# Performance work log

Measured on AMD Instinct MI355X. Metric: run time of the kernel, lower is better.

## Reference

```python
import jax, jax.numpy as jnp
import numpy as np

N_NODES = 50000


def _gcn_norm(edge_index, num_nodes):
    # PyG GCNConv default: add self-loops, symmetric normalization D^-1/2 A D^-1/2
    row, col = edge_index[0], edge_index[1]
    loop = jnp.arange(num_nodes, dtype=edge_index.dtype)
    row = jnp.concatenate([row, loop])
    col = jnp.concatenate([col, loop])
    deg = jax.ops.segment_sum(jnp.ones_like(col, dtype=jnp.float32), col,
                              num_segments=num_nodes)
    deg_inv_sqrt = jnp.where(deg > 0, jax.lax.rsqrt(deg), 0.0)
    norm = deg_inv_sqrt[row] * deg_inv_sqrt[col]  # [E + N]
    return row, col, norm


def _gcn_conv(x, row, col, norm, W, b):
    h = x @ W                                   # [N, out]
    msg = h[row] * norm[:, None]                # gather + scale, [E+N, out]
    out = jax.ops.segment_sum(msg, col, num_segments=x.shape[0])  # scatter-add
    return out + b


def setup_inputs() -> dict:
    key = jax.random.key(0)
    k_x, k_e, k_w1, k_w2 = jax.random.split(key, 4)
    n, e, d = N_NODES, 800000, 64
    x = jax.random.normal(k_x, (n, d), dtype=jnp.float32)
    edge_index = jax.random.randint(k_e, (2, e), 0, n, dtype=jnp.int64)
    # Glorot init like PyG's Linear inside GCNConv (bias separate, zero-init here as randn-small)
    s1 = (6.0 / (d + d)) ** 0.5
    W1 = jax.random.uniform(k_w1, (d, d), jnp.float32, -s1, s1)
    W2 = jax.random.uniform(k_w2, (d, d), jnp.float32, -s1, s1)
    b1 = jnp.zeros((d,), jnp.float32)
    b2 = jnp.zeros((d,), jnp.float32)
    return {"x": x, "edge_index": edge_index, "W1": W1, "b1": b1, "W2": W2, "b2": b2}


def reference(x, edge_index, W1, b1, W2, b2):
    row, col, norm = _gcn_norm(edge_index, x.shape[0])
    h = _gcn_conv(x, row, col, norm, W1, b1)   # layer 1: in -> out
    h = _gcn_conv(h, row, col, norm, W2, b2)   # layer 2: out -> out
    return h
```

## Files before the change

### kernel.cpp

```cpp
#include <hip/hip_runtime.h>
#include <hip/hip_fp16.h>

#define DD 64
#define BSH 6
#define BNODES 64
#define NSUB 8
#define SCAP 256
#define BCAP 1536

__global__ __launch_bounds__(256) void k_zero(int4* __restrict__ p, int n4) {
    int i = blockIdx.x * 256 + threadIdx.x;
    if (i < n4) p[i] = make_int4(0, 0, 0, 0);
}

__global__ __launch_bounds__(256) void k_fill3(const int* __restrict__ rowi,
                                               const int* __restrict__ coli,
                                               int* __restrict__ cur,
                                               unsigned int* __restrict__ pk, int E) {
    int i = blockIdx.x * 256 + threadIdx.x;
    if (i < E) {
        int c = coli[i];
        int idx = (c >> BSH) * NSUB + (blockIdx.x & (NSUB - 1));
        int p = atomicAdd(&cur[idx * 16], 1);
        if (p < SCAP)
            pk[(size_t)idx * SCAP + p] =
                (unsigned int)rowi[i] | ((unsigned int)(c & (BNODES - 1)) << 16);
    }
}

__global__ __launch_bounds__(256) void k_bsort(const int* __restrict__ cur,
                                               const unsigned int* __restrict__ pk,
                                               int* __restrict__ off_s,
                                               int* __restrict__ off_e,
                                               float* __restrict__ dis,
                                               int* __restrict__ srt, int n) {
    __shared__ unsigned int stage[NSUB * SCAP];
    __shared__ int cnt[BNODES];
    __shared__ int cbase[BNODES];
    __shared__ int sb8[NSUB + 1];
    int t = threadIdx.x;
    int b = blockIdx.x;

    if (t < BNODES) cnt[t] = 0;
    if (t < NSUB) {
        int v = cur[(b * NSUB + t) * 16];
        if (v > SCAP) v = SCAP;
        int x = v;
#pragma unroll
        for (int d = 1; d < NSUB; d <<= 1) {
            int u = __shfl_up(x, d, NSUB);
            if ((t & (NSUB - 1)) >= d) x += u;
        }
        sb8[t + 1] = x;
        if (t == 0) sb8[0] = 0;
    }
    __syncthreads();
    int tot = sb8[NSUB];

#pragma unroll
    for (int s = 0; s < NSUB; ++s) {
        int c0 = sb8[s], len = sb8[s + 1] - c0;
        const unsigned int* src = pk + ((size_t)b * NSUB + s) * SCAP;
        for (int i = t; i < len; i += 256) stage[c0 + i] = src[i];
    }
    __syncthreads();

    for (int i = t; i < tot; i += 256) atomicAdd(&cnt[stage[i] >> 16], 1);
    __syncthreads();

    if (t < BNODES) {
        int v = cnt[t], x = v;
#pragma unroll
        for (int d = 1; d < 64; d <<= 1) {
            int u = __shfl_up(x, d);
            if (t >= d) x += u;
        }
        int excl = x - v;
        cbase[t] = excl;
        int c = b * BNODES + t;
        if (c < n) {
            off_s[c] = b * BCAP + excl;
            off_e[c] = b * BCAP + excl + v;
            dis[c] = rsqrtf((float)(v + 1));
        }
    }
    __syncthreads();

    int sbeg = b * BCAP;
    for (int i = t; i < tot; i += 256) {
        unsigned int k = stage[i];
        int pos = atomicAdd(&cbase[k >> 16], 1);
        srt[sbeg + pos] = (int)(k & 0xFFFFu);
    }
}

__global__ __launch_bounds__(64) void k_mm(const float* __restrict__ X,
                                           const float* __restrict__ W,
                                           const float* __restrict__ dis,
                                           __half* __restrict__ H, int n) {
    int lane  = threadIdx.x;
    int tile  = blockIdx.x >> 1;
    int jbase = (blockIdx.x & 1) * 32;
    int r     = tile * 64 + lane;
    int rc    = min(r, n - 1);

    const float4* X4 = (const float4*)X;
    float acc[32];
#pragma unroll
    for (int j = 0; j < 32; ++j) acc[j] = 0.f;

#pragma unroll 1
    for (int kc = 0; kc < 16; ++kc) {
        float4 xv = X4[(size_t)rc * 16 + kc];
        const float* W0 = W + (kc * 4) * 64 + jbase;
#pragma unroll
        for (int u = 0; u < 4; ++u) {
            float xk = (u == 0) ? xv.x : (u == 1) ? xv.y : (u == 2) ? xv.z : xv.w;
            const float* Wk = W0 + u * 64;
#pragma unroll
            for (int j = 0; j < 32; ++j)
                acc[j] = fmaf(xk, Wk[j], acc[j]);
        }
    }
    if (r < n) {
        float d = dis[r];
        __half2 hh[16];
#pragma unroll
        for (int q = 0; q < 16; ++q)
            hh[q] = __floats2half2_rn(acc[2 * q] * d, acc[2 * q + 1] * d);
        uint4* dst = (uint4*)(H + (size_t)r * DD + jbase);
        const uint4* src = (const uint4*)hh;
#pragma unroll
        for (int q = 0; q < 4; ++q) dst[q] = src[q];
    }
}

__global__ __launch_bounds__(256) void k_agg(const int* __restrict__ off_s,
                                             const int* __restrict__ off_e,
                                             const int* __restrict__ srt,
                                             const float* __restrict__ dis,
                                             const __half* __restrict__ hs,
                                             const float* __restrict__ bias,
                                             float* __restrict__ out, int n) {
    int lane = threadIdx.x & 63;
    int j    = lane & 31;
    int hsel = lane >> 5;
    int c = __builtin_amdgcn_readfirstlane(blockIdx.x * 4 + (threadIdx.x >> 6));
    if (c >= n) return;

    int s = __builtin_amdgcn_readfirstlane(off_s[c]);
    int e = __builtin_amdgcn_readfirstlane(off_e[c]);

    const __half2* hs2 = (const __half2*)hs;

    float ax = 0.f, ay = 0.f;
    if (hsel == 0) {
        float2 f = __half22float2(hs2[(size_t)c * 32 + j]);
        ax = f.x; ay = f.y;
    }

    int p = s;
    for (; p + 8 <= e; p += 8) {
        int r0 = srt[p + 0], r1 = srt[p + 1], r2 = srt[p + 2], r3 = srt[p + 3];
        int r4 = srt[p + 4], r5 = srt[p + 5], r6 = srt[p + 6], r7 = srt[p + 7];
        int ra = hsel ? r1 : r0;
        int rb = hsel ? r3 : r2;
        int rg = hsel ? r5 : r4;
        int rd = hsel ? r7 : r6;
        float2 f0 = __half22float2(hs2[(size_t)ra * 32 + j]);
        float2 f1 = __half22float2(hs2[(size_t)rb * 32 + j]);
        float2 f2 = __half22float2(hs2[(size_t)rg * 32 + j]);
        float2 f3 = __half22float2(hs2[(size_t)rd * 32 + j]);
        ax += (f0.x + f1.x) + (f2.x + f3.x);
        ay += (f0.y + f1.y) + (f2.y + f3.y);
    }
    for (; p + 2 <= e; p += 2) {
        int r0 = srt[p], r1 = srt[p + 1];
        int ra = hsel ? r1 : r0;
        float2 f = __half22float2(hs2[(size_t)ra * 32 + j]);
        ax += f.x; ay += f.y;
    }
    if (p < e && hsel == 0) {
        float2 f = __half22float2(hs2[(size_t)srt[p] * 32 + j]);
        ax += f.x; ay += f.y;
    }

    ax += __shfl_xor(ax, 32);
    ay += __shfl_xor(ay, 32);

    if (hsel == 0) {
        float d = dis[c];
        float2 bb = ((const float2*)bias)[j];
        float2 o;
        o.x = bb.x + d * ax;
        o.y = bb.y + d * ay;
        ((float2*)out)[(size_t)c * 32 + j] = o;
    }
}

extern "C" void kernel_launch(void* const* d_in, const int* in_sizes, int n_in,
                              void* d_out, int out_size, void* d_ws, size_t ws_size,
                              hipStream_t stream) {
    const float* x  = (const float*)d_in[0];
    const int*   ei = (const int*)d_in[1];
    const float* W1 = (const float*)d_in[2];
    const float* b1 = (const float*)d_in[3];
    const float* W2 = (const float*)d_in[4];
    const float* b2 = (const float*)d_in[5];
    float* out = (float*)d_out;

    int n = in_sizes[0] / DD;
    int E = in_sizes[1] / 2;
    const int* rowi = ei;
    const int* coli = ei + E;
    int nb = (n + BNODES - 1) / BNODES;
    int M  = nb * NSUB;

    char* ws = (char*)d_ws;
    int*          cur   = (int*)ws;
    int*          off_s = (int*)(ws + (size_t)512 * 1024);
    int*          off_e = (int*)(ws + (size_t)768 * 1024);
    float*        dis   = (float*)(ws + (size_t)1024 * 1024);
    unsigned int* pk    = (unsigned int*)(ws + (size_t)1536 * 1024);
    int*          srt   = (int*)(ws + (size_t)8192 * 1024);
    __half*       hs    = (__half*)(ws + (size_t)13312 * 1024);
    float*        o1    = out;

    int n4    = M * 16 / 4;
    int nb_z  = (n4 + 255) / 256;
    int nb_e  = (E + 255) / 256;
    int nb_mm = ((n + 63) / 64) * 2;
    int nb_ag = (n + 3) / 4;

    k_zero <<<nb_z, 256, 0, stream>>>((int4*)cur, n4);
    k_fill3<<<nb_e, 256, 0, stream>>>(rowi, coli, cur, pk, E);
    k_bsort<<<nb, 256, 0, stream>>>(cur, pk, off_s, off_e, dis, srt, n);

    k_mm <<<nb_mm, 64, 0, stream>>>(x, W1, dis, hs, n);
    k_agg<<<nb_ag, 256, 0, stream>>>(off_s, off_e, srt, dis, hs, b1, o1, n);

    k_mm <<<nb_mm, 64, 0, stream>>>(o1, W2, dis, hs, n);
    k_agg<<<nb_ag, 256, 0, stream>>>(off_s, off_e, srt, dis, hs, b2, out, n);
}
```

Measured before the change: 130.3 us.

## Fuse aggregation and matmul per layer by aggregating before the transform

Uses linearity to reorder each GCN layer from A(XW) to (AX)W. Each layer's neighbour aggregation and 64x64 matmul now run in one 1024-thread kernel that holds the aggregated block in LDS. The first layer's half-precision, deg-scaled input is produced at the end of the bucket-sort kernel, and layer 1 emits the scaled half input for layer 2 directly. This removes the separate matmul launches and the global round trip of the intermediate features. The cost is large blocks with LDS use and W read from global in the inner loop, with half rounding now applied to the raw inputs rather than to XW.

Result: slower. 169.2 us (+29.8%).

```diff
diff --git a/kernel.cpp b/kernel.cpp
--- a/kernel.cpp
+++ b/kernel.cpp
@@ -7,6 +7,7 @@
 #define NSUB 8
 #define SCAP 256
 #define BCAP 1536
+#define SSTR 65
 
 __global__ __launch_bounds__(256) void k_zero(int4* __restrict__ p, int n4) {
     int i = blockIdx.x * 256 + threadIdx.x;
@@ -33,11 +34,14 @@
                                                int* __restrict__ off_s,
                                                int* __restrict__ off_e,
                                                float* __restrict__ dis,
-                                               int* __restrict__ srt, int n) {
+                                               int* __restrict__ srt,
+                                               const float* __restrict__ x,
+                                               __half* __restrict__ xh, int n) {
     __shared__ unsigned int stage[NSUB * SCAP];
     __shared__ int cnt[BNODES];
     __shared__ int cbase[BNODES];
     __shared__ int sb8[NSUB + 1];
+    __shared__ float sdis[BNODES];
     int t = threadIdx.x;
     int b = blockIdx.x;
 
@@ -45,13 +49,13 @@
     if (t < NSUB) {
         int v = cur[(b * NSUB + t) * 16];
         if (v > SCAP) v = SCAP;
-        int x = v;
+        int xs = v;
 #pragma unroll
         for (int d = 1; d < NSUB; d <<= 1) {
-            int u = __shfl_up(x, d, NSUB);
-            if ((t & (NSUB - 1)) >= d) x += u;
-        }
-        sb8[t + 1] = x;
+            int u = __shfl_up(xs, d, NSUB);
+            if ((t & (NSUB - 1)) >= d) xs += u;
+        }
+        sb8[t + 1] = xs;
         if (t == 0) sb8[0] = 0;
     }
     __syncthreads();
@@ -69,19 +73,21 @@
     __syncthreads();
 
     if (t < BNODES) {
-        int v = cnt[t], x = v;
+        int v = cnt[t], xx = v;
 #pragma unroll
         for (int d = 1; d < 64; d <<= 1) {
-            int u = __shfl_up(x, d);
-            if (t >= d) x += u;
-        }
-        int excl = x - v;
+            int u = __shfl_up(xx, d);
+            if (t >= d) xx += u;
+        }
+        int excl = xx - v;
         cbase[t] = excl;
+        float dv = rsqrtf((float)(v + 1));
+        sdis[t] = dv;
         int c = b * BNODES + t;
         if (c < n) {
             off_s[c] = b * BCAP + excl;
             off_e[c] = b * BCAP + excl + v;
-            dis[c] = rsqrtf((float)(v + 1));
+            dis[c]   = dv;
         }
     }
     __syncthreads();
@@ -92,109 +98,112 @@
         int pos = atomicAdd(&cbase[k >> 16], 1);
         srt[sbeg + pos] = (int)(k & 0xFFFFu);
     }
-}
-
-__global__ __launch_bounds__(64) void k_mm(const float* __restrict__ X,
-                                           const float* __restrict__ W,
-                                           const float* __restrict__ dis,
-                                           __half* __restrict__ H, int n) {
-    int lane  = threadIdx.x;
-    int tile  = blockIdx.x >> 1;
-    int jbase = (blockIdx.x & 1) * 32;
-    int r     = tile * 64 + lane;
-    int rc    = min(r, n - 1);
-
-    const float4* X4 = (const float4*)X;
-    float acc[32];
-#pragma unroll
-    for (int j = 0; j < 32; ++j) acc[j] = 0.f;
-
-#pragma unroll 1
-    for (int kc = 0; kc < 16; ++kc) {
-        float4 xv = X4[(size_t)rc * 16 + kc];
-        const float* W0 = W + (kc * 4) * 64 + jbase;
-#pragma unroll
-        for (int u = 0; u < 4; ++u) {
-            float xk = (u == 0) ? xv.x : (u == 1) ? xv.y : (u == 2) ? xv.z : xv.w;
-            const float* Wk = W0 + u * 64;
-#pragma unroll
-            for (int j = 0; j < 32; ++j)
-                acc[j] = fmaf(xk, Wk[j], acc[j]);
-        }
-    }
-    if (r < n) {
-        float d = dis[r];
-        __half2 hh[16];
-#pragma unroll
-        for (int q = 0; q < 16; ++q)
-            hh[q] = __floats2half2_rn(acc[2 * q] * d, acc[2 * q + 1] * d);
-        uint4* dst = (uint4*)(H + (size_t)r * DD + jbase);
-        const uint4* src = (const uint4*)hh;
-#pragma unroll
-        for (int q = 0; q < 4; ++q) dst[q] = src[q];
-    }
-}
-
-__global__ __launch_bounds__(256) void k_agg(const int* __restrict__ off_s,
-                                             const int* __restrict__ off_e,
-                                             const int* __restrict__ srt,
-                                             const float* __restrict__ dis,
-                                             const __half* __restrict__ hs,
-                                             const float* __restrict__ bias,
-                                             float* __restrict__ out, int n) {
-    int lane = threadIdx.x & 63;
-    int j    = lane & 31;
-    int hsel = lane >> 5;
-    int c = __builtin_amdgcn_readfirstlane(blockIdx.x * 4 + (threadIdx.x >> 6));
-    if (c >= n) return;
-
-    int s = __builtin_amdgcn_readfirstlane(off_s[c]);
-    int e = __builtin_amdgcn_readfirstlane(off_e[c]);
-
-    const __half2* hs2 = (const __half2*)hs;
-
-    float ax = 0.f, ay = 0.f;
-    if (hsel == 0) {
-        float2 f = __half22float2(hs2[(size_t)c * 32 + j]);
-        ax = f.x; ay = f.y;
-    }
-
-    int p = s;
-    for (; p + 8 <= e; p += 8) {
-        int r0 = srt[p + 0], r1 = srt[p + 1], r2 = srt[p + 2], r3 = srt[p + 3];
-        int r4 = srt[p + 4], r5 = srt[p + 5], r6 = srt[p + 6], r7 = srt[p + 7];
-        int ra = hsel ? r1 : r0;
-        int rb = hsel ? r3 : r2;
-        int rg = hsel ? r5 : r4;
-        int rd = hsel ? r7 : r6;
-        float2 f0 = __half22float2(hs2[(size_t)ra * 32 + j]);
-        float2 f1 = __half22float2(hs2[(size_t)rb * 32 + j]);
-        float2 f2 = __half22float2(hs2[(size_t)rg * 32 + j]);
-        float2 f3 = __half22float2(hs2[(size_t)rd * 32 + j]);
-        ax += (f0.x + f1.x) + (f2.x + f3.x);
-        ay += (f0.y + f1.y) + (f2.y + f3.y);
-    }
-    for (; p + 2 <= e; p += 2) {
-        int r0 = srt[p], r1 = srt[p + 1];
-        int ra = hsel ? r1 : r0;
-        float2 f = __half22float2(hs2[(size_t)ra * 32 + j]);
-        ax += f.x; ay += f.y;
-    }
-    if (p < e && hsel == 0) {
-        float2 f = __half22float2(hs2[(size_t)srt[p] * 32 + j]);
-        ax += f.x; ay += f.y;
-    }
-
-    ax += __shfl_xor(ax, 32);
-    ay += __shfl_xor(ay, 32);
-
-    if (hsel == 0) {
-        float d = dis[c];
-        float2 bb = ((const float2*)bias)[j];
-        float2 o;
-        o.x = bb.x + d * ax;
-        o.y = bb.y + d * ay;
-        ((float2*)out)[(size_t)c * 32 + j] = o;
+
+    int wv = t >> 6, lane = t & 63;
+    for (int i = wv; i < BNODES; i += 4) {
+        int c = b * BNODES + i;
+        if (c < n)
+            xh[(size_t)c * DD + lane] = __float2half(sdis[i] * x[(size_t)c * DD + lane]);
+    }
+}
+
+__global__ __launch_bounds__(1024) void k_layer(const int* __restrict__ off_s,
+                                                const int* __restrict__ off_e,
+                                                const int* __restrict__ srt,
+                                                const float* __restrict__ dis,
+                                                const __half* __restrict__ xh,
+                                                const float* __restrict__ W,
+                                                const float* __restrict__ bias,
+                                                float* __restrict__ out,
+                                                __half* __restrict__ xh_next,
+                                                int n) {
+    __shared__ float s_lds[BNODES * SSTR];
+    const int t    = threadIdx.x;
+    const int wv   = t >> 6;
+    const int lane = t & 63;
+    const int j    = lane & 31;
+    const int hsel = lane >> 5;
+    const int b    = blockIdx.x;
+    const int c0   = b * BNODES;
+    const __half2* hs2 = (const __half2*)xh;
+
+    for (int i = wv; i < BNODES; i += 16) {
+        int cc = c0 + i;
+        if (cc < n) {
+            int c = __builtin_amdgcn_readfirstlane(cc);
+            int s = __builtin_amdgcn_readfirstlane(off_s[c]);
+            int e = __builtin_amdgcn_readfirstlane(off_e[c]);
+
+            float ax = 0.f, ay = 0.f;
+            if (hsel == 0) {
+                float2 f = __half22float2(hs2[(size_t)c * 32 + j]);
+                ax = f.x; ay = f.y;
+            }
+            int p = s;
+            for (; p + 8 <= e; p += 8) {
+                int r0 = srt[p + 0], r1 = srt[p + 1], r2 = srt[p + 2], r3 = srt[p + 3];
+                int r4 = srt[p + 4], r5 = srt[p + 5], r6 = srt[p + 6], r7 = srt[p + 7];
+                int ra = hsel ? r1 : r0;
+                int rb = hsel ? r3 : r2;
+                int rg = hsel ? r5 : r4;
+                int rd = hsel ? r7 : r6;
+                float2 f0 = __half22float2(hs2[(size_t)ra * 32 + j]);
+                float2 f1 = __half22float2(hs2[(size_t)rb * 32 + j]);
+                float2 f2 = __half22float2(hs2[(size_t)rg * 32 + j]);
+                float2 f3 = __half22float2(hs2[(size_t)rd * 32 + j]);
+                ax += (f0.x + f1.x) + (f2.x + f3.x);
+                ay += (f0.y + f1.y) + (f2.y + f3.y);
+            }
+            for (; p + 2 <= e; p += 2) {
+                int r0 = srt[p], r1 = srt[p + 1];
+                int ra = hsel ? r1 : r0;
+                float2 f = __half22float2(hs2[(size_t)ra * 32 + j]);
+                ax += f.x; ay += f.y;
+            }
+            if (p < e && hsel == 0) {
+                float2 f = __half22float2(hs2[(size_t)srt[p] * 32 + j]);
+                ax += f.x; ay += f.y;
+            }
+            ax += __shfl_xor(ax, 32);
+            ay += __shfl_xor(ay, 32);
+            if (hsel == 0) {
+                float d = dis[c];
+                s_lds[i * SSTR + 2 * j]     = d * ax;
+                s_lds[i * SSTR + 2 * j + 1] = d * ay;
+            }
+        }
+    }
+    __syncthreads();
+
+    const int jbase = wv * 4;
+    const int r = lane;
+    const int c = c0 + r;
+    float a0 = 0.f, a1 = 0.f, a2 = 0.f, a3 = 0.f;
+#pragma unroll 8
+    for (int k = 0; k < 64; ++k) {
+        float sk = s_lds[r * SSTR + k];
+        const float* Wk = W + k * 64 + jbase;
+        a0 = fmaf(sk, Wk[0], a0);
+        a1 = fmaf(sk, Wk[1], a1);
+        a2 = fmaf(sk, Wk[2], a2);
+        a3 = fmaf(sk, Wk[3], a3);
+    }
+    if (c < n) {
+        float4 o;
+        o.x = a0 + bias[jbase + 0];
+        o.y = a1 + bias[jbase + 1];
+        o.z = a2 + bias[jbase + 2];
+        o.w = a3 + bias[jbase + 3];
+        *(float4*)(out + (size_t)c * DD + jbase) = o;
+        if (xh_next) {
+            float dn = dis[c];
+            __half2 h0 = __floats2half2_rn(o.x * dn, o.y * dn);
+            __half2 h1 = __floats2half2_rn(o.z * dn, o.w * dn);
+            uint2 pack;
+            pack.x = *(const unsigned int*)&h0;
+            pack.y = *(const unsigned int*)&h1;
+            *(uint2*)(xh_next + (size_t)c * DD + jbase) = pack;
+        }
     }
 }
 
@@ -223,22 +232,18 @@
     float*        dis   = (float*)(ws + (size_t)1024 * 1024);
     unsigned int* pk    = (unsigned int*)(ws + (size_t)1536 * 1024);
     int*          srt   = (int*)(ws + (size_t)8192 * 1024);
-    __half*       hs    = (__half*)(ws + (size_t)13312 * 1024);
-    float*        o1    = out;
-
-    int n4    = M * 16 / 4;
-    int nb_z  = (n4 + 255) / 256;
-    int nb_e  = (E + 255) / 256;
-    int nb_mm = ((n + 63) / 64) * 2;
-    int nb_ag = (n + 3) / 4;
+    __half*       xh    = (__half*)(ws + (size_t)13312 * 1024);
+    __half*       xh2   = (__half*)(ws + (size_t)20480 * 1024);
+
+    int n4   = M * 16 / 4;
+    int nb_z = (n4 + 255) / 256;
+    int nb_e = (E + 255) / 256;
 
     k_zero <<<nb_z, 256, 0, stream>>>((int4*)cur, n4);
     k_fill3<<<nb_e, 256, 0, stream>>>(rowi, coli, cur, pk, E);
-    k_bsort<<<nb, 256, 0, stream>>>(cur, pk, off_s, off_e, dis, srt, n);
-
-    k_mm <<<nb_mm, 64, 0, stream>>>(x, W1, dis, hs, n);
-    k_agg<<<nb_ag, 256, 0, stream>>>(off_s, off_e, srt, dis, hs, b1, o1, n);
-
-    k_mm <<<nb_mm, 64, 0, stream>>>(o1, W2, dis, hs, n);
-    k_agg<<<nb_ag, 256, 0, stream>>>(off_s, off_e, srt, dis, hs, b2, out, n);
-}
+    k_bsort<<<nb, 256, 0, stream>>>(cur, pk, off_s, off_e, dis, srt, x, xh, n);
+
+    k_layer<<<nb, 1024, 0, stream>>>(off_s, off_e, srt, dis, xh, W1, b1, out, xh2, n);
+
+    k_layer<<<nb, 1024, 0, stream>>>(off_s, off_e, srt, dis, xh2, W2, b2, out, (void*)0 ? xh2 : (__half*)nullptr, n);
+}
```
